# Optimization experiments

Measured on AMD Instinct MI355X. Metric: run time of the kernel, lower is better.

The kernel has to match this reference:

```python
import jax, jax.numpy as jnp
import numpy as np

NUM_ITERATIONS = 3


def squash(x, axis):
    # squared_norm/(1+squared_norm) * x / sqrt(squared_norm), as in the torch module
    sn = jnp.sum(x * x, axis=axis, keepdims=True)
    return sn / (1.0 + sn) * x / jnp.sqrt(sn)


def setup_inputs() -> dict:
    key = jax.random.key(0)
    k1, k2 = jax.random.split(key)
    batch, num_caps, num_route, in_ch, out_ch = 32, 32, 4608, 8, 16
    x = jax.random.normal(k1, (batch, num_route, in_ch), dtype=jnp.float32)
    route_weights = jax.random.normal(k2, (num_caps, num_route, in_ch, out_ch), dtype=jnp.float32)
    return {"x": x, "route_weights": route_weights}


def reference(x, route_weights):
    # U[b,c,r,1,o] = x[b,1,r,1,i] @ W[1,c,r,i,o]
    U = jnp.einsum("bri,crio->bcro", x, route_weights)[:, :, :, None, :]  # [b,c,r,1,o]
    B = jnp.zeros_like(U)
    V = None
    for _ in range(NUM_ITERATIONS):
        C = jax.nn.softmax(B, axis=1)                 # softmax over capsules
        S = jnp.sum(C * U, axis=2, keepdims=True)      # reduce over route nodes: [b,c,1,1,o]
        V = squash(S, axis=-1)
        B = B + U * V
    b, c = B.shape[0], B.shape[1]
    o = B.shape[-1]
    return V.reshape(b, c, o)
```

## Files before the change

kernel.cpp:

```cpp
#include <hip/hip_runtime.h>

#define BATCH 32
#define NCAPS 32
#define NR    4608
#define NI    8
#define NO    16
#define CSTR  200
#define MAXRB 36
#define L2E   1.44269504088896341f

typedef float f2 __attribute__((ext_vector_type(2)));

template<int RB, bool FIRST>
__global__ __launch_bounds__(1024, 4) void caps_route_fast(
    const float* __restrict__ x,
    const float* __restrict__ W,
    const float* __restrict__ A,
    float* __restrict__ P)
{
    __shared__ __align__(16) float Ws[2][NCAPS * CSTR];
    __shared__ __align__(16) f2    xP[RB][BATCH / 2][NI + 1];

    const int t  = threadIdx.x;
    const int cq = t & 3;
    const int o  = (t >> 2) & 15;
    const int w  = t >> 6;
    const int b0 = 2 * w;
    const int r0 = blockIdx.x * RB;

    f2 a2[8];
    if (!FIRST) {
#pragma unroll
        for (int cl = 0; cl < 8; ++cl) {
            a2[cl].x = A[((b0 + 0) * NCAPS + 8 * cq + cl) * NO + o] * L2E;
            a2[cl].y = A[((b0 + 1) * NCAPS + 8 * cq + cl) * NO + o] * L2E;
        }
    }
    f2 acc[8];
#pragma unroll
    for (int cl = 0; cl < 8; ++cl) acc[cl] = (f2)0.f;

    for (int s = t; s < RB * (BATCH / 2); s += 1024) {
        const int rr = s >> 4, bp = s & 15;
        const float* xp0 = &x[((size_t)(2 * bp + 0) * NR + r0 + rr) * NI];
        const float* xp1 = &x[((size_t)(2 * bp + 1) * NR + r0 + rr) * NI];
        const float4 a0 = *(const float4*)xp0;
        const float4 a1 = *(const float4*)(xp0 + 4);
        const float4 c0 = *(const float4*)xp1;
        const float4 c1 = *(const float4*)(xp1 + 4);
        f2* d = &xP[rr][bp][0];
        d[0] = f2{a0.x, c0.x}; d[1] = f2{a0.y, c0.y};
        d[2] = f2{a0.z, c0.z}; d[3] = f2{a0.w, c0.w};
        d[4] = f2{a1.x, c1.x}; d[5] = f2{a1.y, c1.y};
        d[6] = f2{a1.z, c1.z}; d[7] = f2{a1.w, c1.w};
    }

    const int c_st = t >> 5;
    const int sl   = 4 * (c_st & 7) + (c_st >> 3);
    const int part = t & 31;
    const int i_st = part >> 2;
    const int o0   = (part & 3) * 4;
    const float* wsrc = W + ((size_t)c_st * NR + r0) * (NI * NO) + part * 4;

    {
        const float4 s0 = *(const float4*)wsrc;
        float* d = &Ws[0][sl * CSTR + o0 * 12 + i_st];
        d[0] = s0.x; d[12] = s0.y; d[24] = s0.z; d[36] = s0.w;
    }
    float4 pf = {};
    if (RB > 1) pf = *(const float4*)(wsrc + NI * NO);
    __syncthreads();

#pragma unroll 1
    for (int rr = 0; rr < RB; ++rr) {
        const int cur = rr & 1;

        if (rr + 1 < RB) {
            float* d = &Ws[cur ^ 1][sl * CSTR + o0 * 12 + i_st];
            d[0] = pf.x; d[12] = pf.y; d[24] = pf.z; d[36] = pf.w;
            if (rr + 2 < RB)
                pf = *(const float4*)(wsrc + (size_t)(rr + 2) * (NI * NO));
        }

        f2 xq[NI];
        {
            const f2* xv = &xP[rr][w][0];
#pragma unroll
            for (int i = 0; i < NI; ++i) xq[i] = xv[i];
        }

        const float* wb = &Ws[cur][cq * CSTR + o * 12];
        if (FIRST) {
#pragma unroll
            for (int cl = 0; cl < 8; ++cl) {
                const float* wp = wb + cl * (4 * CSTR);
                const float4 w0 = *(const float4*)wp;
                const float4 w1 = *(const float4*)(wp + 4);
                f2 u2 = xq[0] * w0.x;
                u2 += xq[1] * w0.y;
                u2 += xq[2] * w0.z;
                u2 += xq[3] * w0.w;
                u2 += xq[4] * w1.x;
                u2 += xq[5] * w1.y;
                u2 += xq[6] * w1.z;
                u2 += xq[7] * w1.w;
                acc[cl] += u2;
            }
        } else {
            f2 tt[8];
            f2 Z = (f2)0.f;
#pragma unroll
            for (int cl = 0; cl < 8; ++cl) {
                const float* wp = wb + cl * (4 * CSTR);
                const float4 w0 = *(const float4*)wp;
                const float4 w1 = *(const float4*)(wp + 4);
                f2 u2 = xq[0] * w0.x;
                u2 += xq[1] * w0.y;
                u2 += xq[2] * w0.z;
                u2 += xq[3] * w0.w;
                u2 += xq[4] * w1.x;
                u2 += xq[5] * w1.y;
                u2 += xq[6] * w1.z;
                u2 += xq[7] * w1.w;
                const f2 l2 = u2 * a2[cl];
                f2 e2;
                e2.x = exp2f(l2.x);
                e2.y = exp2f(l2.y);
                Z += e2;
                tt[cl] = e2 * u2;
            }
            Z.x += __shfl_xor(Z.x, 1); Z.x += __shfl_xor(Z.x, 2);
            Z.y += __shfl_xor(Z.y, 1); Z.y += __shfl_xor(Z.y, 2);
            f2 rz;
            rz.x = __builtin_amdgcn_rcpf(Z.x);
            rz.y = __builtin_amdgcn_rcpf(Z.y);
#pragma unroll
            for (int cl = 0; cl < 8; ++cl)
                acc[cl] += tt[cl] * rz;
        }
        __syncthreads();
    }

#pragma unroll
    for (int bb = 0; bb < 2; ++bb) {
        float* pout = P + (((size_t)blockIdx.x * BATCH + b0 + bb) * NO + o) * NCAPS + 8 * cq;
        float4 v0, v1;
        v0.x = bb ? acc[0].y : acc[0].x; v0.y = bb ? acc[1].y : acc[1].x;
        v0.z = bb ? acc[2].y : acc[2].x; v0.w = bb ? acc[3].y : acc[3].x;
        v1.x = bb ? acc[4].y : acc[4].x; v1.y = bb ? acc[5].y : acc[5].x;
        v1.z = bb ? acc[6].y : acc[6].x; v1.w = bb ? acc[7].y : acc[7].x;
        if (FIRST) {
            v0.x *= 0.03125f; v0.y *= 0.03125f; v0.z *= 0.03125f; v0.w *= 0.03125f;
            v1.x *= 0.03125f; v1.y *= 0.03125f; v1.z *= 0.03125f; v1.w *= 0.03125f;
        }
        *(float4*)pout = v0;
        *(float4*)(pout + 4) = v1;
    }
}

__global__ __launch_bounds__(256) void caps_partial(const float* __restrict__ P,
                                                    float* __restrict__ P2)
{
    const int tid = threadIdx.x;
    const int ct  = blockIdx.x & 15;
    const int rg  = blockIdx.x >> 4;
    const size_t col = (size_t)ct * 1024 + tid * 4;
    const float* p = P + (size_t)rg * 16 * 16384 + col;
    float4 s = {0.f, 0.f, 0.f, 0.f};
#pragma unroll
    for (int k = 0; k < 16; ++k) {
        const float4 v = *(const float4*)(p + (size_t)k * 16384);
        s.x += v.x; s.y += v.y; s.z += v.z; s.w += v.w;
    }
    *(float4*)(P2 + (size_t)rg * 16384 + col) = s;
}

__global__ void caps_reduce_squash(const float* __restrict__ P,
                                   float* __restrict__ A,
                                   float* __restrict__ out,
                                   int nchunk)
{
    __shared__ float sm[256];
    const int bc  = blockIdx.x;
    const int b   = bc >> 5;
    const int c   = bc & 31;
    const int tid = threadIdx.x;
    const int o = tid & 15;
    const int j = tid >> 4;
    float s = 0.f;
    for (int tch = j; tch < nchunk; tch += 16)
        s += P[(((size_t)tch * BATCH + b) * NO + o) * NCAPS + c];
    sm[tid] = s;
    __syncthreads();
    if (tid < 16) {
        float S = 0.f;
#pragma unroll
        for (int k = 0; k < 16; ++k) S += sm[tid + 16 * k];
        float sq = S * S;
#pragma unroll
        for (int d = 8; d >= 1; d >>= 1) sq += __shfl_xor(sq, d, 16);
        const float scale = sq / ((1.f + sq) * sqrtf(sq));
        const float V = S * scale;
        const int idx = bc * NO + tid;
        A[idx] += V;
        if (out) out[idx] = V;
    }
}

__global__ __launch_bounds__(512, 2) void caps_route_generic(
    const float* __restrict__ x, const float* __restrict__ W,
    const float* __restrict__ A, float* __restrict__ P, int rb)
{
    __shared__ __align__(16) float Ws[NCAPS * CSTR];
    __shared__ __align__(16) float xsT[NI * MAXRB * BATCH];

    const int t = threadIdx.x;
    const int b = t & 31;
    const int o = t >> 5;
    const int r0 = blockIdx.x * rb;
    const int rbs = rb * BATCH;

    float a2s[NCAPS];
#pragma unroll
    for (int c = 0; c < NCAPS; ++c)
        a2s[c] = A[(b * NCAPS + c) * NO + o] * L2E;
    float acc[NCAPS];
#pragma unroll
    for (int c = 0; c < NCAPS; ++c) acc[c] = 0.f;

    for (int s = t; s < rbs; s += 512) {
        const int rr = s >> 5, bb = s & 31;
        const float4 v0 = *(const float4*)&x[((size_t)bb * NR + r0 + rr) * NI];
        const float4 v1 = *(const float4*)&x[((size_t)bb * NR + r0 + rr) * NI + 4];
        const float tmp[8] = {v0.x, v0.y, v0.z, v0.w, v1.x, v1.y, v1.z, v1.w};
#pragma unroll
        for (int i = 0; i < NI; ++i) xsT[i * rbs + s] = tmp[i];
    }

    const int cs  = t >> 4;
    const int seg = t & 15;
    const int iw  = seg >> 1;
    const int ob  = (seg & 1) * 8;
    const float* wsrc = W + ((size_t)cs * NR + r0) * (NI * NO) + seg * 8;
    float4 pf0 = *(const float4*)wsrc;
    float4 pf1 = *(const float4*)(wsrc + 4);

    for (int rr = 0; rr < rb; ++rr) {
        __syncthreads();
        {
            const float tmp[8] = {pf0.x, pf0.y, pf0.z, pf0.w,
                                  pf1.x, pf1.y, pf1.z, pf1.w};
#pragma unroll
            for (int k = 0; k < 8; ++k)
                Ws[cs * CSTR + (ob + k) * 12 + iw] = tmp[k];
        }
        if (rr + 1 < rb) {
            wsrc += NI * NO;
            pf0 = *(const float4*)wsrc;
            pf1 = *(const float4*)(wsrc + 4);
        }
        __syncthreads();

        float xq[NI];
#pragma unroll
        for (int i = 0; i < NI; ++i) xq[i] = xsT[i * rbs + rr * 32 + b];

        float tt[NCAPS];
        float Z = 0.f;
        const float* bp = &Ws[o * 12];
#pragma unroll
        for (int c = 0; c < NCAPS; ++c) {
            const float* wp = bp + c * CSTR;
            const float4 w0 = *(const float4*)wp;
            const float4 w1 = *(const float4*)(wp + 4);
            float uu =      xq[0] * w0.x;
            uu = fmaf(xq[1], w0.y, uu);
            uu = fmaf(xq[2], w0.z, uu);
            uu = fmaf(xq[3], w0.w, uu);
            uu = fmaf(xq[4], w1.x, uu);
            uu = fmaf(xq[5], w1.y, uu);
            uu = fmaf(xq[6], w1.z, uu);
            uu = fmaf(xq[7], w1.w, uu);
            const float ee = exp2f(uu * a2s[c]);
            Z += ee;
            tt[c] = ee * uu;
        }
        const float rz = __builtin_amdgcn_rcpf(Z);
#pragma unroll
        for (int c = 0; c < NCAPS; ++c)
            acc[c] = fmaf(tt[c], rz, acc[c]);
    }

    float* pout = P + (((size_t)blockIdx.x * BATCH + b) * NO + o) * NCAPS;
#pragma unroll
    for (int q = 0; q < NCAPS / 4; ++q) {
        float4 v;
        v.x = acc[4 * q + 0]; v.y = acc[4 * q + 1];
        v.z = acc[4 * q + 2]; v.w = acc[4 * q + 3];
        *(float4*)(pout + 4 * q) = v;
    }
}

__global__ void caps_zero(float* __restrict__ p, int n)
{
    const int i = blockIdx.x * blockDim.x + threadIdx.x;
    if (i < n) p[i] = 0.f;
}

extern "C" void kernel_launch(void* const* d_in, const int* in_sizes, int n_in,
                              void* d_out, int out_size, void* d_ws, size_t ws_size,
                              hipStream_t stream)
{
    const float* x = (const float*)d_in[0];
    const float* W = (const float*)d_in[1];
    float* out = (float*)d_out;

    float* A  = (float*)d_ws;
    float* P  = A + BATCH * NCAPS * NO;
    float* P2 = P + (size_t)256 * BATCH * NCAPS * NO;

    const size_t elem = (size_t)BATCH * NCAPS * NO;
    caps_zero<<<(int)((elem + 255) / 256), 256, 0, stream>>>(A, (int)elem);

    if ((1 + 256 + 16) * elem * sizeof(float) <= ws_size) {
        caps_route_fast<18, true><<<256, 1024, 0, stream>>>(x, W, A, P);
        caps_partial<<<256, 256, 0, stream>>>(P, P2);
        caps_reduce_squash<<<BATCH * NCAPS, 256, 0, stream>>>(P2, A, nullptr, 16);
        caps_route_fast<18, false><<<256, 1024, 0, stream>>>(x, W, A, P);
        caps_partial<<<256, 256, 0, stream>>>(P, P2);
        caps_reduce_squash<<<BATCH * NCAPS, 256, 0, stream>>>(P2, A, nullptr, 16);
        caps_route_fast<18, false><<<256, 1024, 0, stream>>>(x, W, A, P);
        caps_partial<<<256, 256, 0, stream>>>(P, P2);
        caps_reduce_squash<<<BATCH * NCAPS, 256, 0, stream>>>(P2, A, out, 16);
    } else {
        int nchunk = 128;
        while (nchunk > 32 &&
               (size_t)(nchunk + 1) * elem * sizeof(float) > ws_size)
            nchunk >>= 1;
        const int rb = NR / nchunk;
        for (int it = 0; it < 3; ++it) {
            caps_route_generic<<<nchunk, 512, 0, stream>>>(x, W, A, P, rb);
            caps_reduce_squash<<<BATCH * NCAPS, 256, 0, stream>>>(
                P, A, it == 2 ? out : nullptr, nchunk);
        }
    }
}
```

Baseline: 154.2 us.

## Remap routing threads to 4 batches by 4 capsules for register reuse

Reassigns thread work in the routing kernel so each thread covers 4 batch entries and 4 capsules instead of 2 batches and 8 capsules. Each W value loaded from shared memory is reused across twice as many batch entries, which halves LDS weight reads per FMA, while x reads double. The softmax denominator now needs a 3-step cross-lane shuffle reduction across capsule groups instead of 2 steps. The launch-bounds occupancy hint drops from 4 to 2 blocks, allowing more registers per thread at the cost of possible lower occupancy.

```diff
diff --git a/kernel.cpp b/kernel.cpp
--- a/kernel.cpp
+++ b/kernel.cpp
@@ -12,35 +12,43 @@
 typedef float f2 __attribute__((ext_vector_type(2)));
 
 template<int RB, bool FIRST>
-__global__ __launch_bounds__(1024, 4) void caps_route_fast(
+__global__ __launch_bounds__(1024, 2) void caps_route_fast(
     const float* __restrict__ x,
     const float* __restrict__ W,
     const float* __restrict__ A,
     float* __restrict__ P)
 {
     __shared__ __align__(16) float Ws[2][NCAPS * CSTR];
-    __shared__ __align__(16) f2    xP[RB][BATCH / 2][NI + 1];
+    __shared__ __align__(16) f2    xP[RB][8][2][NI];
 
     const int t  = threadIdx.x;
-    const int cq = t & 3;
-    const int o  = (t >> 2) & 15;
+    const int om = (t & 3) | (((t >> 3) & 1) << 2);
+    const int co = ((t >> 4) & 1) | (((t >> 2) & 1) << 1) | (((t >> 5) & 1) << 2);
     const int w  = t >> 6;
-    const int b0 = 2 * w;
+    const int oh = w & 1;
+    const int bq = w >> 1;
+    const int o  = oh * 8 + om;
+    const int b0 = 4 * bq;
     const int r0 = blockIdx.x * RB;
 
-    f2 a2[8];
+    f2 a2[2][4];
     if (!FIRST) {
 #pragma unroll
-        for (int cl = 0; cl < 8; ++cl) {
-            a2[cl].x = A[((b0 + 0) * NCAPS + 8 * cq + cl) * NO + o] * L2E;
-            a2[cl].y = A[((b0 + 1) * NCAPS + 8 * cq + cl) * NO + o] * L2E;
-        }
-    }
-    f2 acc[8];
-#pragma unroll
-    for (int cl = 0; cl < 8; ++cl) acc[cl] = (f2)0.f;
-
-    for (int s = t; s < RB * (BATCH / 2); s += 1024) {
+        for (int p = 0; p < 2; ++p)
+#pragma unroll
+            for (int cl = 0; cl < 4; ++cl) {
+                const int c = 4 * co + cl;
+                a2[p][cl].x = A[((b0 + 2 * p + 0) * NCAPS + c) * NO + o] * L2E;
+                a2[p][cl].y = A[((b0 + 2 * p + 1) * NCAPS + c) * NO + o] * L2E;
+            }
+    }
+    f2 acc[2][4];
+#pragma unroll
+    for (int p = 0; p < 2; ++p)
+#pragma unroll
+        for (int cl = 0; cl < 4; ++cl) acc[p][cl] = (f2)0.f;
+
+    for (int s = t; s < RB * 16; s += 1024) {
         const int rr = s >> 4, bp = s & 15;
         const float* xp0 = &x[((size_t)(2 * bp + 0) * NR + r0 + rr) * NI];
         const float* xp1 = &x[((size_t)(2 * bp + 1) * NR + r0 + rr) * NI];
@@ -48,7 +56,7 @@
         const float4 a1 = *(const float4*)(xp0 + 4);
         const float4 c0 = *(const float4*)xp1;
         const float4 c1 = *(const float4*)(xp1 + 4);
-        f2* d = &xP[rr][bp][0];
+        f2* d = &xP[rr][bp >> 1][bp & 1][0];
         d[0] = f2{a0.x, c0.x}; d[1] = f2{a0.y, c0.y};
         d[2] = f2{a0.z, c0.z}; d[3] = f2{a0.w, c0.w};
         d[4] = f2{a1.x, c1.x}; d[5] = f2{a1.y, c1.y};
@@ -56,7 +64,7 @@
     }
 
     const int c_st = t >> 5;
-    const int sl   = 4 * (c_st & 7) + (c_st >> 3);
+    const int sl   = (c_st >> 2) + 8 * (c_st & 3);
     const int part = t & 31;
     const int i_st = part >> 2;
     const int o0   = (part & 3) * 4;
@@ -82,79 +90,95 @@
                 pf = *(const float4*)(wsrc + (size_t)(rr + 2) * (NI * NO));
         }
 
-        f2 xq[NI];
+        f2 xq[2][NI];
         {
-            const f2* xv = &xP[rr][w][0];
-#pragma unroll
-            for (int i = 0; i < NI; ++i) xq[i] = xv[i];
-        }
-
-        const float* wb = &Ws[cur][cq * CSTR + o * 12];
+            const f2* xv = &xP[rr][bq][0][0];
+#pragma unroll
+            for (int i = 0; i < NI; ++i) { xq[0][i] = xv[i]; xq[1][i] = xv[NI + i]; }
+        }
+
+        const float* wb = &Ws[cur][co * CSTR + o * 12];
         if (FIRST) {
 #pragma unroll
-            for (int cl = 0; cl < 8; ++cl) {
-                const float* wp = wb + cl * (4 * CSTR);
+            for (int cl = 0; cl < 4; ++cl) {
+                const float* wp = wb + cl * (8 * CSTR);
                 const float4 w0 = *(const float4*)wp;
                 const float4 w1 = *(const float4*)(wp + 4);
-                f2 u2 = xq[0] * w0.x;
-                u2 += xq[1] * w0.y;
-                u2 += xq[2] * w0.z;
-                u2 += xq[3] * w0.w;
-                u2 += xq[4] * w1.x;
-                u2 += xq[5] * w1.y;
-                u2 += xq[6] * w1.z;
-                u2 += xq[7] * w1.w;
-                acc[cl] += u2;
+#pragma unroll
+                for (int p = 0; p < 2; ++p) {
+                    f2 u2 = xq[p][0] * w0.x;
+                    u2 += xq[p][1] * w0.y;
+                    u2 += xq[p][2] * w0.z;
+                    u2 += xq[p][3] * w0.w;
+                    u2 += xq[p][4] * w1.x;
+                    u2 += xq[p][5] * w1.y;
+                    u2 += xq[p][6] * w1.z;
+                    u2 += xq[p][7] * w1.w;
+                    acc[p][cl] += u2;
+                }
             }
         } else {
-            f2 tt[8];
-            f2 Z = (f2)0.f;
-#pragma unroll
-            for (int cl = 0; cl < 8; ++cl) {
-                const float* wp = wb + cl * (4 * CSTR);
+            f2 tt[2][4];
+            f2 Z0 = (f2)0.f, Z1 = (f2)0.f;
+#pragma unroll
+            for (int cl = 0; cl < 4; ++cl) {
+                const float* wp = wb + cl * (8 * CSTR);
                 const float4 w0 = *(const float4*)wp;
                 const float4 w1 = *(const float4*)(wp + 4);
-                f2 u2 = xq[0] * w0.x;
-                u2 += xq[1] * w0.y;
-                u2 += xq[2] * w0.z;
-                u2 += xq[3] * w0.w;
-                u2 += xq[4] * w1.x;
-                u2 += xq[5] * w1.y;
-                u2 += xq[6] * w1.z;
-                u2 += xq[7] * w1.w;
-                const f2 l2 = u2 * a2[cl];
-                f2 e2;
-                e2.x = exp2f(l2.x);
-                e2.y = exp2f(l2.y);
-                Z += e2;
-                tt[cl] = e2 * u2;
-            }
-            Z.x += __shfl_xor(Z.x, 1); Z.x += __shfl_xor(Z.x, 2);
-            Z.y += __shfl_xor(Z.y, 1); Z.y += __shfl_xor(Z.y, 2);
-            f2 rz;
-            rz.x = __builtin_amdgcn_rcpf(Z.x);
-            rz.y = __builtin_amdgcn_rcpf(Z.y);
-#pragma unroll
-            for (int cl = 0; cl < 8; ++cl)
-                acc[cl] += tt[cl] * rz;
+                f2 u0 = xq[0][0] * w0.x;
+                u0 += xq[0][1] * w0.y;
+                u0 += xq[0][2] * w0.z;
+                u0 += xq[0][3] * w0.w;
+                u0 += xq[0][4] * w1.x;
+                u0 += xq[0][5] * w1.y;
+                u0 += xq[0][6] * w1.z;
+                u0 += xq[0][7] * w1.w;
+                f2 u1 = xq[1][0] * w0.x;
+                u1 += xq[1][1] * w0.y;
+                u1 += xq[1][2] * w0.z;
+                u1 += xq[1][3] * w0.w;
+                u1 += xq[1][4] * w1.x;
+                u1 += xq[1][5] * w1.y;
+                u1 += xq[1][6] * w1.z;
+                u1 += xq[1][7] * w1.w;
+                const f2 l0 = u0 * a2[0][cl];
+                const f2 l1 = u1 * a2[1][cl];
+                f2 e0, e1;
+                e0.x = exp2f(l0.x); e0.y = exp2f(l0.y);
+                e1.x = exp2f(l1.x); e1.y = exp2f(l1.y);
+                Z0 += e0; Z1 += e1;
+                tt[0][cl] = e0 * u0;
+                tt[1][cl] = e1 * u1;
+            }
+#pragma unroll
+            for (int m = 0; m < 3; ++m) {
+                const int msk = (m == 0) ? 4 : (m == 1) ? 16 : 32;
+                Z0.x += __shfl_xor(Z0.x, msk); Z0.y += __shfl_xor(Z0.y, msk);
+                Z1.x += __shfl_xor(Z1.x, msk); Z1.y += __shfl_xor(Z1.y, msk);
+            }
+            f2 rz0, rz1;
+            rz0.x = __builtin_amdgcn_rcpf(Z0.x); rz0.y = __builtin_amdgcn_rcpf(Z0.y);
+            rz1.x = __builtin_amdgcn_rcpf(Z1.x); rz1.y = __builtin_amdgcn_rcpf(Z1.y);
+#pragma unroll
+            for (int cl = 0; cl < 4; ++cl) {
+                acc[0][cl] += tt[0][cl] * rz0;
+                acc[1][cl] += tt[1][cl] * rz1;
+            }
         }
         __syncthreads();
     }
 
 #pragma unroll
-    for (int bb = 0; bb < 2; ++bb) {
-        float* pout = P + (((size_t)blockIdx.x * BATCH + b0 + bb) * NO + o) * NCAPS + 8 * cq;
-        float4 v0, v1;
-        v0.x = bb ? acc[0].y : acc[0].x; v0.y = bb ? acc[1].y : acc[1].x;
-        v0.z = bb ? acc[2].y : acc[2].x; v0.w = bb ? acc[3].y : acc[3].x;
-        v1.x = bb ? acc[4].y : acc[4].x; v1.y = bb ? acc[5].y : acc[5].x;
-        v1.z = bb ? acc[6].y : acc[6].x; v1.w = bb ? acc[7].y : acc[7].x;
-        if (FIRST) {
-            v0.x *= 0.03125f; v0.y *= 0.03125f; v0.z *= 0.03125f; v0.w *= 0.03125f;
-            v1.x *= 0.03125f; v1.y *= 0.03125f; v1.z *= 0.03125f; v1.w *= 0.03125f;
-        }
-        *(float4*)pout = v0;
-        *(float4*)(pout + 4) = v1;
+    for (int bb = 0; bb < 4; ++bb) {
+        const int p = bb >> 1, h = bb & 1;
+        float* pout = P + (((size_t)blockIdx.x * BATCH + b0 + bb) * NO + o) * NCAPS + 4 * co;
+        float4 v;
+        v.x = h ? acc[p][0].y : acc[p][0].x;
+        v.y = h ? acc[p][1].y : acc[p][1].x;
+        v.z = h ? acc[p][2].y : acc[p][2].x;
+        v.w = h ? acc[p][3].y : acc[p][3].x;
+        if (FIRST) { v.x *= 0.03125f; v.y *= 0.03125f; v.z *= 0.03125f; v.w *= 0.03125f; }
+        *(float4*)pout = v;
     }
 }
 
```

Measured after the change: 156.2 us. No clear change (+1.3%).
